# Performance work log

Hardware: AMD Instinct MI355X
Metric: run time of the kernel (lower is better)

## Reference

```python
import jax, jax.numpy as jnp
import numpy as np

EPS = 1e-5
NUM_GROUPS = 32


def setup_inputs() -> dict:
    key = jax.random.key(0)
    B, C, H, W = 16, 512, 32, 32
    ks = jax.random.split(key, 5)
    s = 1.0 / np.sqrt(C)  # keep attention logits well-scaled
    return {
        "x": jax.random.normal(ks[0], (B, C, H, W), jnp.float32),
        "gamma": jnp.ones((C,), jnp.float32),
        "beta": jnp.zeros((C,), jnp.float32),
        "wq": jax.random.normal(ks[1], (C, C), jnp.float32) * s,
        "bq": jnp.zeros((C,), jnp.float32),
        "wk": jax.random.normal(ks[2], (C, C), jnp.float32) * s,
        "bk": jnp.zeros((C,), jnp.float32),
        "wv": jax.random.normal(ks[3], (C, C), jnp.float32) * s,
        "bv": jnp.zeros((C,), jnp.float32),
        "wp": jax.random.normal(ks[4], (C, C), jnp.float32) * s,
        "bp": jnp.zeros((C,), jnp.float32),
    }


def _group_norm(x, gamma, beta):
    B, C, H, W = x.shape
    g = NUM_GROUPS
    xg = x.reshape(B, g, C // g, H * W)
    mu = jnp.mean(xg, axis=(2, 3), keepdims=True)
    var = jnp.mean(jnp.square(xg - mu), axis=(2, 3), keepdims=True)
    h = (xg - mu) * jax.lax.rsqrt(var + EPS)
    h = h.reshape(B, C, H, W)
    return h * gamma[None, :, None, None] + beta[None, :, None, None]


def reference(x, gamma, beta, wq, bq, wk, bk, wv, bv, wp, bp):
    B, C, H, W = x.shape
    N = H * W
    h = _group_norm(x, gamma, beta).reshape(B, C, N)  # [B,C,N]
    # 1x1 convs == per-pixel matmuls over channels
    q = jnp.einsum('oc,bcn->bon', wq, h) + bq[None, :, None]
    k = jnp.einsum('oc,bcn->bon', wk, h) + bk[None, :, None]
    v = jnp.einsum('oc,bcn->bon', wv, h) + bv[None, :, None]
    scale = int(C) ** (-0.5)
    logits = jnp.einsum('bcn,bcm->bnm', q, k) * scale  # [B,N,N]
    attn = jax.nn.softmax(logits, axis=-1)
    o = jnp.einsum('bnm,bcm->bcn', attn, v)  # [B,C,N]
    out = jnp.einsum('oc,bcn->bon', wp, o) + bp[None, :, None]
    return x + out.reshape(B, C, H, W)
```

## Files before the change

kernel.cpp:

```cpp
#include <hip/hip_runtime.h>
#include <hip/hip_bf16.h>

typedef __attribute__((ext_vector_type(8))) short bf16x8;
typedef __attribute__((ext_vector_type(4))) float f32x4;
typedef __attribute__((ext_vector_type(8))) unsigned short u16x8;
typedef __attribute__((ext_vector_type(4))) unsigned short u16x4;

static __device__ __forceinline__ unsigned short f2bf(float f) {
  __hip_bfloat16 h = __float2bfloat16(f);
  union { __hip_bfloat16 h; unsigned short u; } cv; cv.h = h; return cv.u;
}
static __device__ __forceinline__ float bf2f(unsigned short u) {
  union { unsigned int u; float f; } cv; cv.u = ((unsigned int)u) << 16; return cv.f;
}

static __device__ __forceinline__ void gload16(const unsigned short* g, unsigned short* l) {
  __builtin_amdgcn_global_load_lds((const __attribute__((address_space(1))) void*)g,
                                   (__attribute__((address_space(3))) void*)l, 16, 0, 0);
}

#define BK 64

__global__ __launch_bounds__(256, 4) void gemm_bt(
    const unsigned short* __restrict__ A, const unsigned short* __restrict__ Bm,
    long sA, long sB, int lda, int ldb, int K,
    const float* __restrict__ bias, int bias_mode, float post_scale,
    int out_mode, void* __restrict__ D, long sD, int ldd,
    const float* __restrict__ resid)
{
  __shared__ unsigned short lA[128 * BK];
  __shared__ unsigned short lB[128 * BK];
  const int gx = gridDim.x, gy = gridDim.y;
  const int nwg = gx * gy * gridDim.z;
  int orig = blockIdx.x + gx * (blockIdx.y + gy * blockIdx.z);
  int id = (orig & 7) * (nwg >> 3) + (orig >> 3);
  const int bxi = id % gx;
  int rem = id / gx;
  const int byi = rem % gy;
  const int bz = rem / gy;

  const int tid = threadIdx.x, lane = tid & 63, wid = tid >> 6;
  const int l15 = lane & 15, lhi = lane >> 4;
  const int wr = wid >> 1, wc = wid & 1;
  const long bm = (long)byi * 128, bn = (long)bxi * 128;
  const unsigned short* Ab = A + (size_t)bz * sA + (size_t)bm * lda;
  const unsigned short* Bb = Bm + (size_t)bz * sB + (size_t)bn * ldb;
  const int NT = K >> 6;

  f32x4 acc[4][4];
  #pragma unroll
  for (int i = 0; i < 4; ++i)
    #pragma unroll
    for (int j = 0; j < 4; ++j) acc[i][j] = (f32x4){0.f, 0.f, 0.f, 0.f};

  auto stage = [&](int k0) {
    #pragma unroll
    for (int j = 0; j < 4; ++j) {
      int bi = j * 256 + tid;
      int row = bi >> 3, sl = bi & 7;
      int kb = sl ^ (row & 7);
      gload16(Ab + (size_t)row * lda + k0 + kb * 8, &lA[(j * 256 + wid * 64) * 8]);
    }
    #pragma unroll
    for (int j = 0; j < 4; ++j) {
      int bi = j * 256 + tid;
      int row = bi >> 3, sl = bi & 7;
      int kb = sl ^ (row & 7);
      gload16(Bb + (size_t)row * ldb + k0 + kb * 8, &lB[(j * 256 + wid * 64) * 8]);
    }
  };

  for (int t = 0; t < NT; ++t) {
    stage(t * BK);
    __syncthreads();
    #pragma unroll
    for (int s = 0; s < 2; ++s) {
      bf16x8 af[4], bfr[4];
      #pragma unroll
      for (int mi = 0; mi < 4; ++mi) {
        int row = wr * 64 + mi * 16 + l15;
        int sl = (s * 4 + lhi) ^ (row & 7);
        af[mi] = *(const bf16x8*)&lA[row * BK + sl * 8];
      }
      #pragma unroll
      for (int ni = 0; ni < 4; ++ni) {
        int row = wc * 64 + ni * 16 + l15;
        int sl = (s * 4 + lhi) ^ (row & 7);
        bfr[ni] = *(const bf16x8*)&lB[row * BK + sl * 8];
      }
      #pragma unroll
      for (int mi = 0; mi < 4; ++mi)
        #pragma unroll
        for (int ni = 0; ni < 4; ++ni)
          acc[mi][ni] = __builtin_amdgcn_mfma_f32_16x16x32_bf16(af[mi], bfr[ni], acc[mi][ni], 0, 0, 0);
    }
    __syncthreads();
  }

  if (out_mode == 0) {
    #pragma unroll
    for (int mi = 0; mi < 4; ++mi) {
      #pragma unroll
      for (int ni = 0; ni < 4; ++ni) {
        #pragma unroll
        for (int r = 0; r < 4; ++r) {
          long row = bm + wr * 64 + mi * 16 + lhi * 4 + r;
          long col = bn + wc * 64 + ni * 16 + l15;
          float v = acc[mi][ni][r];
          if (bias_mode == 1) v += bias[row];
          else if (bias_mode == 2) v += bias[col];
          v *= post_scale;
          ((unsigned short*)D)[(size_t)bz * sD + (size_t)row * ldd + col] = f2bf(v);
        }
      }
    }
  } else {
    float* outF = (float*)D;
    #pragma unroll
    for (int mi = 0; mi < 4; ++mi) {
      #pragma unroll
      for (int ni = 0; ni < 4; ++ni) {
        #pragma unroll
        for (int r = 0; r < 4; ++r) {
          long row = bm + wr * 64 + mi * 16 + lhi * 4 + r;
          long col = bn + wc * 64 + ni * 16 + l15;
          float v = acc[mi][ni][r];
          if (bias_mode == 1) v += bias[row];
          v *= post_scale;
          size_t oi = (size_t)(col >> 10) * 524288 + (size_t)row * 1024 + (col & 1023);
          outF[oi] = v + resid[oi];
        }
      }
    }
  }
}

__global__ __launch_bounds__(256) void groupnorm_to_ht(
    const float* __restrict__ x, const float* __restrict__ gamma,
    const float* __restrict__ beta, unsigned short* __restrict__ ht)
{
  const int b = blockIdx.x >> 5;
  const int g = blockIdx.x & 31;
  const int tid = threadIdx.x, lane = tid & 63, wid = tid >> 6;
  const float4* xg4 = (const float4*)(x + ((size_t)b * 512 + g * 16) * 1024);
  float4 v[16];
  float s = 0.f, ss = 0.f;
  #pragma unroll
  for (int j = 0; j < 16; ++j) {
    v[j] = xg4[j * 256 + tid];
    s += v[j].x + v[j].y + v[j].z + v[j].w;
    ss += v[j].x * v[j].x + v[j].y * v[j].y + v[j].z * v[j].z + v[j].w * v[j].w;
  }
  #pragma unroll
  for (int o = 32; o; o >>= 1) { s += __shfl_xor(s, o); ss += __shfl_xor(ss, o); }
  __shared__ float red[8];
  if (lane == 0) { red[wid] = s; red[4 + wid] = ss; }
  __syncthreads();
  s = red[0] + red[1] + red[2] + red[3];
  ss = red[4] + red[5] + red[6] + red[7];
  const float mu = s * (1.f / 16384.f);
  const float var = ss * (1.f / 16384.f) - mu * mu;
  const float rsig = rsqrtf(var + 1e-5f);
  __shared__ unsigned short tile[16][1024];
  #pragma unroll
  for (int j = 0; j < 16; ++j) {
    int e = (j * 256 + tid) * 4;
    int ci = e >> 10, n = e & 1023;
    float ga = gamma[g * 16 + ci] * rsig, be = beta[g * 16 + ci];
    u16x4 o = { f2bf((v[j].x - mu) * ga + be), f2bf((v[j].y - mu) * ga + be),
                f2bf((v[j].z - mu) * ga + be), f2bf((v[j].w - mu) * ga + be) };
    *(u16x4*)&tile[ci][n] = o;
  }
  __syncthreads();
  unsigned short* hb = ht + (size_t)b * 1024 * 512 + g * 16;
  for (int rep = 0; rep < 4; ++rep) {
    int n = rep * 256 + tid;
    u16x8 lo, hi;
    #pragma unroll
    for (int ci = 0; ci < 8; ++ci) lo[ci] = tile[ci][n];
    #pragma unroll
    for (int ci = 0; ci < 8; ++ci) hi[ci] = tile[8 + ci][n];
    *(u16x8*)&hb[(size_t)n * 512] = lo;
    *(u16x8*)&hb[(size_t)n * 512 + 8] = hi;
  }
}

__global__ __launch_bounds__(256) void softmax_rows(unsigned short* __restrict__ attn)
{
  int row = blockIdx.x * 4 + (threadIdx.x >> 6);
  int lane = threadIdx.x & 63;
  unsigned short* p = attn + (size_t)row * 1024;
  u16x8 c0 = *(const u16x8*)&p[lane * 8];
  u16x8 c1 = *(const u16x8*)&p[512 + lane * 8];
  float f[16];
  #pragma unroll
  for (int j = 0; j < 8; ++j) { f[j] = bf2f(c0[j]); f[8 + j] = bf2f(c1[j]); }
  float m = f[0];
  #pragma unroll
  for (int j = 1; j < 16; ++j) m = fmaxf(m, f[j]);
  #pragma unroll
  for (int o = 32; o; o >>= 1) m = fmaxf(m, __shfl_xor(m, o));
  float sum = 0.f;
  #pragma unroll
  for (int j = 0; j < 16; ++j) { f[j] = __expf(f[j] - m); sum += f[j]; }
  #pragma unroll
  for (int o = 32; o; o >>= 1) sum += __shfl_xor(sum, o);
  float inv = 1.0f / sum;
  #pragma unroll
  for (int j = 0; j < 8; ++j) { c0[j] = f2bf(f[j] * inv); c1[j] = f2bf(f[8 + j] * inv); }
  *(u16x8*)&p[lane * 8] = c0;
  *(u16x8*)&p[512 + lane * 8] = c1;
}

__global__ __launch_bounds__(256) void convert_weights(
    const float* __restrict__ wq, const float* __restrict__ wk,
    const float* __restrict__ wv, const float* __restrict__ wp,
    const float* __restrict__ bq, const float* __restrict__ bk,
    unsigned short* __restrict__ out, float* __restrict__ bqk)
{
  if (blockIdx.x == 1024) {
    int i = threadIdx.x * 4;
    if (i < 512) *(float4*)&bqk[i] = *(const float4*)&bq[i];
    else         *(float4*)&bqk[i] = *(const float4*)&bk[i - 512];
    return;
  }
  int t = blockIdx.x * 256 + threadIdx.x;
  int m = t >> 16;
  int off = (t & 65535) * 4;
  const float* src = m == 0 ? wq : m == 1 ? wk : m == 2 ? wv : wp;
  float4 v = *(const float4*)&src[off];
  u16x4 o = { f2bf(v.x), f2bf(v.y), f2bf(v.z), f2bf(v.w) };
  *(u16x4*)&out[(size_t)m * 262144 + off] = o;
}

extern "C" void kernel_launch(void* const* d_in, const int* in_sizes, int n_in,
                              void* d_out, int out_size, void* d_ws, size_t ws_size,
                              hipStream_t stream)
{
  const float* x     = (const float*)d_in[0];
  const float* gamma = (const float*)d_in[1];
  const float* beta  = (const float*)d_in[2];
  const float* wq    = (const float*)d_in[3];
  const float* bq    = (const float*)d_in[4];
  const float* wk    = (const float*)d_in[5];
  const float* bk    = (const float*)d_in[6];
  const float* wv    = (const float*)d_in[7];
  const float* bv    = (const float*)d_in[8];
  const float* wp    = (const float*)d_in[9];
  const float* bp    = (const float*)d_in[10];

  unsigned short* ws   = (unsigned short*)d_ws;
  unsigned short* w_bf = ws;
  unsigned short* ht   = w_bf + 1048576;
  unsigned short* qk   = ht + 8388608;
  unsigned short* vv2  = qk + 16777216;
  unsigned short* attn = vv2 + 8388608;
  unsigned short* ot   = attn + 16777216;
  float*          bqk  = (float*)(ot + 8388608);

  const float scale = 0.044194173824159216f;

  convert_weights<<<dim3(1025), dim3(256), 0, stream>>>(wq, wk, wv, wp, bq, bk, w_bf, bqk);
  groupnorm_to_ht<<<dim3(512), dim3(256), 0, stream>>>(x, gamma, beta, ht);

  gemm_bt<<<dim3(8, 128, 1), dim3(256), 0, stream>>>(
      ht, w_bf, 0L, 0L, 512, 512, 512,
      bqk, 2, 1.0f, 0, (void*)qk, 0L, 1024, (const float*)nullptr);
  gemm_bt<<<dim3(128, 4, 1), dim3(256), 0, stream>>>(
      w_bf + 2 * 262144, ht, 0L, 0L, 512, 512, 512,
      bv, 1, 1.0f, 0, (void*)vv2, 0L, 16384, (const float*)nullptr);
  gemm_bt<<<dim3(8, 8, 16), dim3(256), 0, stream>>>(
      qk, qk + 512, 1048576L, 1048576L, 1024, 1024, 512,
      (const float*)nullptr, 0, scale, 0, (void*)attn, 1048576L, 1024, (const float*)nullptr);
  softmax_rows<<<dim3(4096), dim3(256), 0, stream>>>(attn);
  gemm_bt<<<dim3(4, 8, 16), dim3(256), 0, stream>>>(
      attn, vv2, 1048576L, 1024L, 1024, 16384, 1024,
      (const float*)nullptr, 0, 1.0f, 0, (void*)ot, 524288L, 512, (const float*)nullptr);
  gemm_bt<<<dim3(128, 4, 1), dim3(256), 0, stream>>>(
      w_bf + 3 * 262144, ot, 0L, 0L, 512, 512, 512,
      bp, 1, 1.0f, 1, d_out, 0L, 16384, x);
}
```

Before: 174.7 us.

## Register-prefetch GEMM tiles and stage epilogue through LDS for vectorized stores

Replaces direct global-to-LDS loads with register prefetch of the next K tile, issued right after the current tile is written to LDS, so global latency overlaps the MFMA work. The epilogue now writes accumulators into padded shared memory and then emits coalesced 16-byte stores, including float4 residual adds, instead of scattered scalar stores. Occupancy hint drops from 4 to 3 blocks and shared memory grows for the epilogue buffer. This adds register pressure and extra barriers.

After: 191.7 us. 9.7% more time.

```diff
diff --git a/kernel.cpp b/kernel.cpp
--- a/kernel.cpp
+++ b/kernel.cpp
@@ -14,22 +14,19 @@
   union { unsigned int u; float f; } cv; cv.u = ((unsigned int)u) << 16; return cv.f;
 }
 
-static __device__ __forceinline__ void gload16(const unsigned short* g, unsigned short* l) {
-  __builtin_amdgcn_global_load_lds((const __attribute__((address_space(1))) void*)g,
-                                   (__attribute__((address_space(3))) void*)l, 16, 0, 0);
-}
-
 #define BK 64
 
-__global__ __launch_bounds__(256, 4) void gemm_bt(
+__global__ __launch_bounds__(256, 3) void gemm_bt(
     const unsigned short* __restrict__ A, const unsigned short* __restrict__ Bm,
     long sA, long sB, int lda, int ldb, int K,
     const float* __restrict__ bias, int bias_mode, float post_scale,
     int out_mode, void* __restrict__ D, long sD, int ldd,
     const float* __restrict__ resid)
 {
-  __shared__ unsigned short lA[128 * BK];
-  __shared__ unsigned short lB[128 * BK];
+  __shared__ __align__(16) unsigned char smem[33792];
+  unsigned short* lA = (unsigned short*)smem;
+  unsigned short* lB = (unsigned short*)(smem + 16384);
+
   const int gx = gridDim.x, gy = gridDim.y;
   const int nwg = gx * gy * gridDim.z;
   int orig = blockIdx.x + gx * (blockIdx.y + gy * blockIdx.z);
@@ -53,26 +50,31 @@
     #pragma unroll
     for (int j = 0; j < 4; ++j) acc[i][j] = (f32x4){0.f, 0.f, 0.f, 0.f};
 
-  auto stage = [&](int k0) {
+  bf16x8 rgA[4], rgB[4];
+  auto issue = [&](int k0) {
     #pragma unroll
     for (int j = 0; j < 4; ++j) {
       int bi = j * 256 + tid;
       int row = bi >> 3, sl = bi & 7;
       int kb = sl ^ (row & 7);
-      gload16(Ab + (size_t)row * lda + k0 + kb * 8, &lA[(j * 256 + wid * 64) * 8]);
-    }
+      rgA[j] = *(const bf16x8*)(Ab + (size_t)row * lda + k0 + kb * 8);
+      rgB[j] = *(const bf16x8*)(Bb + (size_t)row * ldb + k0 + kb * 8);
+    }
+  };
+
+  issue(0);
+  for (int t = 0; t < NT; ++t) {
+    asm volatile("s_waitcnt lgkmcnt(0)" ::: "memory");
+    __builtin_amdgcn_s_barrier();
     #pragma unroll
     for (int j = 0; j < 4; ++j) {
-      int bi = j * 256 + tid;
-      int row = bi >> 3, sl = bi & 7;
-      int kb = sl ^ (row & 7);
-      gload16(Bb + (size_t)row * ldb + k0 + kb * 8, &lB[(j * 256 + wid * 64) * 8]);
-    }
-  };
-
-  for (int t = 0; t < NT; ++t) {
-    stage(t * BK);
-    __syncthreads();
+      *(bf16x8*)&lA[(j * 256 + tid) * 8] = rgA[j];
+      *(bf16x8*)&lB[(j * 256 + tid) * 8] = rgB[j];
+    }
+    asm volatile("s_waitcnt lgkmcnt(0)" ::: "memory");
+    __builtin_amdgcn_s_barrier();
+    __builtin_amdgcn_sched_barrier(0);
+    if (t + 1 < NT) issue((t + 1) * BK);
     #pragma unroll
     for (int s = 0; s < 2; ++s) {
       bf16x8 af[4], bfr[4];
@@ -94,43 +96,71 @@
         for (int ni = 0; ni < 4; ++ni)
           acc[mi][ni] = __builtin_amdgcn_mfma_f32_16x16x32_bf16(af[mi], bfr[ni], acc[mi][ni], 0, 0, 0);
     }
-    __syncthreads();
-  }
+  }
+  __syncthreads();
 
   if (out_mode == 0) {
-    #pragma unroll
-    for (int mi = 0; mi < 4; ++mi) {
-      #pragma unroll
-      for (int ni = 0; ni < 4; ++ni) {
+    unsigned short* ep = (unsigned short*)smem;
+    #pragma unroll
+    for (int p = 0; p < 2; ++p) {
+      if (wr == p) {
         #pragma unroll
-        for (int r = 0; r < 4; ++r) {
-          long row = bm + wr * 64 + mi * 16 + lhi * 4 + r;
-          long col = bn + wc * 64 + ni * 16 + l15;
-          float v = acc[mi][ni][r];
-          if (bias_mode == 1) v += bias[row];
-          else if (bias_mode == 2) v += bias[col];
-          v *= post_scale;
-          ((unsigned short*)D)[(size_t)bz * sD + (size_t)row * ldd + col] = f2bf(v);
-        }
-      }
+        for (int mi = 0; mi < 4; ++mi)
+          #pragma unroll
+          for (int ni = 0; ni < 4; ++ni)
+            #pragma unroll
+            for (int r = 0; r < 4; ++r) {
+              int rl = mi * 16 + lhi * 4 + r;
+              int cl = wc * 64 + ni * 16 + l15;
+              float v = acc[mi][ni][r];
+              if (bias_mode == 1) v += bias[bm + p * 64 + rl];
+              else if (bias_mode == 2) v += bias[bn + cl];
+              ep[rl * 136 + cl] = f2bf(v * post_scale);
+            }
+      }
+      __syncthreads();
+      #pragma unroll
+      for (int it = 0; it < 4; ++it) {
+        int c = it * 256 + tid;
+        int row = c >> 4, pos = c & 15;
+        unsigned short* dst = (unsigned short*)D + (size_t)bz * sD
+                            + (size_t)(bm + p * 64 + row) * ldd + bn + pos * 8;
+        *(u16x8*)dst = *(const u16x8*)&ep[row * 136 + pos * 8];
+      }
+      __syncthreads();
     }
   } else {
+    float* smf = (float*)smem;
     float* outF = (float*)D;
-    #pragma unroll
-    for (int mi = 0; mi < 4; ++mi) {
-      #pragma unroll
-      for (int ni = 0; ni < 4; ++ni) {
+    const long b_ = bn >> 10, n0 = bn & 1023;
+    #pragma unroll
+    for (int p = 0; p < 2; ++p) {
+      if (wr == p) {
         #pragma unroll
-        for (int r = 0; r < 4; ++r) {
-          long row = bm + wr * 64 + mi * 16 + lhi * 4 + r;
-          long col = bn + wc * 64 + ni * 16 + l15;
-          float v = acc[mi][ni][r];
-          if (bias_mode == 1) v += bias[row];
-          v *= post_scale;
-          size_t oi = (size_t)(col >> 10) * 524288 + (size_t)row * 1024 + (col & 1023);
-          outF[oi] = v + resid[oi];
-        }
-      }
+        for (int mi = 0; mi < 4; ++mi)
+          #pragma unroll
+          for (int ni = 0; ni < 4; ++ni)
+            #pragma unroll
+            for (int r = 0; r < 4; ++r) {
+              int rl = mi * 16 + lhi * 4 + r;
+              int cl = wc * 64 + ni * 16 + l15;
+              float v = acc[mi][ni][r];
+              if (bias_mode == 1) v += bias[bm + p * 64 + rl];
+              smf[rl * 132 + cl] = v * post_scale;
+            }
+      }
+      __syncthreads();
+      #pragma unroll
+      for (int it = 0; it < 8; ++it) {
+        int c = it * 256 + tid;
+        int row = c >> 5, pos = c & 31;
+        size_t oi = (size_t)b_ * 524288 + (size_t)(bm + p * 64 + row) * 1024 + n0 + pos * 4;
+        float4 v = *(const float4*)&smf[row * 132 + pos * 4];
+        float4 xr = *(const float4*)&resid[oi];
+        float4 o = { v.x + xr.x, v.y + xr.y, v.z + xr.z, v.w + xr.w };
+        *(float4*)&outF[oi] = o;
+      }
+      __syncthreads();
     }
   }
 }
```

## Split GEMM into producer and consumer waves with double-buffered LDS

Applied to the files above, without the earlier changes.

The GEMM block doubles to 512 threads. Waves 0-3 only issue global-to-LDS loads into a second buffer for the next K tile, while waves 4-7 run MFMAs on the current one; raw s_barriers keep the two groups in step. This is meant to hide global load latency behind compute instead of serialising load, sync and compute each iteration. In exchange, LDS per block doubles to 64KB, which cuts blocks per CU, and half the waves do little work. Producer waves return early, so any barrier left in the epilogue would be unsafe.

New measurement: 189.3 us. +8.3%, slower.

```diff
diff --git a/kernel.cpp b/kernel.cpp
--- a/kernel.cpp
+++ b/kernel.cpp
@@ -21,15 +21,15 @@
 
 #define BK 64
 
-__global__ __launch_bounds__(256, 4) void gemm_bt(
+__global__ __launch_bounds__(512, 4) void gemm_bt(
     const unsigned short* __restrict__ A, const unsigned short* __restrict__ Bm,
     long sA, long sB, int lda, int ldb, int K,
     const float* __restrict__ bias, int bias_mode, float post_scale,
     int out_mode, void* __restrict__ D, long sD, int ldd,
     const float* __restrict__ resid)
 {
-  __shared__ unsigned short lA[128 * BK];
-  __shared__ unsigned short lB[128 * BK];
+  __shared__ unsigned short lA[2][128 * BK];
+  __shared__ unsigned short lB[2][128 * BK];
   const int gx = gridDim.x, gy = gridDim.y;
   const int nwg = gx * gy * gridDim.z;
   int orig = blockIdx.x + gx * (blockIdx.y + gy * blockIdx.z);
@@ -41,38 +41,52 @@
 
   const int tid = threadIdx.x, lane = tid & 63, wid = tid >> 6;
   const int l15 = lane & 15, lhi = lane >> 4;
-  const int wr = wid >> 1, wc = wid & 1;
+  const int cw = wid & 3;
+  const int wr = cw >> 1, wc = cw & 1;
   const long bm = (long)byi * 128, bn = (long)bxi * 128;
   const unsigned short* Ab = A + (size_t)bz * sA + (size_t)bm * lda;
   const unsigned short* Bb = Bm + (size_t)bz * sB + (size_t)bn * ldb;
   const int NT = K >> 6;
 
+  if (wid < 4) {
+    auto stage = [&](int buf, int k0) {
+      #pragma unroll
+      for (int j = 0; j < 4; ++j) {
+        int bi = j * 256 + tid;
+        int row = bi >> 3, sl = bi & 7;
+        int kb = sl ^ (row & 7);
+        gload16(Ab + (size_t)row * lda + k0 + kb * 8, &lA[buf][(j * 256 + wid * 64) * 8]);
+      }
+      #pragma unroll
+      for (int j = 0; j < 4; ++j) {
+        int bi = j * 256 + tid;
+        int row = bi >> 3, sl = bi & 7;
+        int kb = sl ^ (row & 7);
+        gload16(Bb + (size_t)row * ldb + k0 + kb * 8, &lB[buf][(j * 256 + wid * 64) * 8]);
+      }
+    };
+    stage(0, 0);
+    asm volatile("s_waitcnt vmcnt(0)" ::: "memory");
+    __builtin_amdgcn_s_barrier();
+    for (int t = 0; t < NT; ++t) {
+      if (t + 1 < NT) {
+        stage((t + 1) & 1, (t + 1) * BK);
+        asm volatile("s_waitcnt vmcnt(0)" ::: "memory");
+      }
+      __builtin_amdgcn_s_barrier();
+    }
+    return;
+  }
+
   f32x4 acc[4][4];
   #pragma unroll
   for (int i = 0; i < 4; ++i)
     #pragma unroll
     for (int j = 0; j < 4; ++j) acc[i][j] = (f32x4){0.f, 0.f, 0.f, 0.f};
 
-  auto stage = [&](int k0) {
-    #pragma unroll
-    for (int j = 0; j < 4; ++j) {
-      int bi = j * 256 + tid;
-      int row = bi >> 3, sl = bi & 7;
-      int kb = sl ^ (row & 7);
-      gload16(Ab + (size_t)row * lda + k0 + kb * 8, &lA[(j * 256 + wid * 64) * 8]);
-    }
-    #pragma unroll
-    for (int j = 0; j < 4; ++j) {
-      int bi = j * 256 + tid;
-      int row = bi >> 3, sl = bi & 7;
-      int kb = sl ^ (row & 7);
-      gload16(Bb + (size_t)row * ldb + k0 + kb * 8, &lB[(j * 256 + wid * 64) * 8]);
-    }
-  };
-
+  __builtin_amdgcn_s_barrier();
   for (int t = 0; t < NT; ++t) {
-    stage(t * BK);
-    __syncthreads();
+    const int buf = t & 1;
     #pragma unroll
     for (int s = 0; s < 2; ++s) {
       bf16x8 af[4], bfr[4];
@@ -80,13 +94,13 @@
       for (int mi = 0; mi < 4; ++mi) {
         int row = wr * 64 + mi * 16 + l15;
         int sl = (s * 4 + lhi) ^ (row & 7);
-        af[mi] = *(const bf16x8*)&lA[row * BK + sl * 8];
+        af[mi] = *(const bf16x8*)&lA[buf][row * BK + sl * 8];
       }
       #pragma unroll
       for (int ni = 0; ni < 4; ++ni) {
         int row = wc * 64 + ni * 16 + l15;
         int sl = (s * 4 + lhi) ^ (row & 7);
-        bfr[ni] = *(const bf16x8*)&lB[row * BK + sl * 8];
+        bfr[ni] = *(const bf16x8*)&lB[buf][row * BK + sl * 8];
       }
       #pragma unroll
       for (int mi = 0; mi < 4; ++mi)
@@ -94,7 +108,8 @@
         for (int ni = 0; ni < 4; ++ni)
           acc[mi][ni] = __builtin_amdgcn_mfma_f32_16x16x32_bf16(af[mi], bfr[ni], acc[mi][ni], 0, 0, 0);
     }
-    __syncthreads();
+    asm volatile("s_waitcnt lgkmcnt(0)" ::: "memory");
+    __builtin_amdgcn_s_barrier();
   }
 
   if (out_mode == 0) {
@@ -263,20 +278,20 @@
   convert_weights<<<dim3(1025), dim3(256), 0, stream>>>(wq, wk, wv, wp, bq, bk, w_bf, bqk);
   groupnorm_to_ht<<<dim3(512), dim3(256), 0, stream>>>(x, gamma, beta, ht);
 
-  gemm_bt<<<dim3(8, 128, 1), dim3(256), 0, stream>>>(
+  gemm_bt<<<dim3(8, 128, 1), dim3(512), 0, stream>>>(
       ht, w_bf, 0L, 0L, 512, 512, 512,
       bqk, 2, 1.0f, 0, (void*)qk, 0L, 1024, (const float*)nullptr);
-  gemm_bt<<<dim3(128, 4, 1), dim3(256), 0, stream>>>(
+  gemm_bt<<<dim3(128, 4, 1), dim3(512), 0, stream>>>(
       w_bf + 2 * 262144, ht, 0L, 0L, 512, 512, 512,
       bv, 1, 1.0f, 0, (void*)vv2, 0L, 16384, (const float*)nullptr);
-  gemm_bt<<<dim3(8, 8, 16), dim3(256), 0, stream>>>(
+  gemm_bt<<<dim3(8, 8, 16), dim3(512), 0, stream>>>(
       qk, qk + 512, 1048576L, 1048576L, 1024, 1024, 512,
       (const float*)nullptr, 0, scale, 0, (void*)attn, 1048576L, 1024, (const float*)nullptr);
   softmax_rows<<<dim3(4096), dim3(256), 0, stream>>>(attn);
-  gemm_bt<<<dim3(4, 8, 16), dim3(256), 0, stream>>>(
+  gemm_bt<<<dim3(4, 8, 16), dim3(512), 0, stream>>>(
       attn, vv2, 1048576L, 1024L, 1024, 16384, 1024,
       (const float*)nullptr, 0, 1.0f, 0, (void*)ot, 524288L, 512, (const float*)nullptr);
-  gemm_bt<<<dim3(128, 4, 1), dim3(256), 0, stream>>>(
+  gemm_bt<<<dim3(128, 4, 1), dim3(512), 0, stream>>>(
       w_bf + 3 * 262144, ot, 0L, 0L, 512, 512, 512,
       bp, 1, 1.0f, 1, d_out, 0L, 16384, x);
 }
```
